# Kernel optimization log

Hardware: AMD Instinct MI355X
Metric: run time of the kernel (lower is better)

## Reference

```python
import jax, jax.numpy as jnp
import numpy as np

N = 100000   # n_nodes
E = 1600000  # n_edges (avg degree 16)
IN, HID, OUT = 128, 128, 64


def setup_inputs() -> dict:
    key = jax.random.key(0)
    k0, k1, k2, k3 = jax.random.split(key, 4)
    x = jax.random.normal(k0, (N, IN), dtype=jnp.float32)
    edge_index = jax.random.randint(k1, (2, E), 0, N, dtype=jnp.int32)
    # Glorot-ish init for GCNConv weights, zero bias (PyG default bias=True)
    W1 = jax.random.normal(k2, (IN, HID), dtype=jnp.float32) * (1.0 / np.sqrt(IN))
    b1 = jnp.zeros((HID,), dtype=jnp.float32)
    W2 = jax.random.normal(k3, (HID, OUT), dtype=jnp.float32) * (1.0 / np.sqrt(HID))
    b2 = jnp.zeros((OUT,), dtype=jnp.float32)
    return {"x": x, "W1": W1, "b1": b1, "W2": W2, "b2": b2, "edge_index": edge_index}


def gcn_layer(x, W, b, src, dst):
    """PyG GCNConv: add self-loops, symmetric deg^{-1/2} normalization,
    linear transform, scatter-add aggregation at dst, plus bias."""
    n = x.shape[0]
    h = x @ W                                   # [n, d_out]
    loops = jnp.arange(n, dtype=src.dtype)
    s = jnp.concatenate([src, loops])           # sources incl. self-loops
    d = jnp.concatenate([dst, loops])           # targets incl. self-loops
    deg = jax.ops.segment_sum(jnp.ones_like(d, dtype=h.dtype), d, num_segments=n)
    dinv = jnp.where(deg > 0, jax.lax.rsqrt(deg), 0.0)
    norm = dinv[s] * dinv[d]                    # [E+n]
    msg = h[s] * norm[:, None]                  # gather + scale
    out = jax.ops.segment_sum(msg, d, num_segments=n)  # scatter-add
    return out + b


def reference(x, W1, b1, W2, b2, edge_index):
    src, dst = edge_index[0], edge_index[1]
    h = jax.nn.relu(gcn_layer(x, W1, b1, src, dst))
    return gcn_layer(h, W2, b2, src, dst)
```

## Files before the change

kernel.cpp:

```cpp
#include <hip/hip_runtime.h>

#define NNODES 100000
#define NEDGES 1600000
#define IND 128
#define HIDD 128
#define OUTD 64

#define BSHIFT 9
#define BSIZE  512
#define NBUCK  ((NNODES + BSIZE - 1) / BSIZE)
#define HIST_EPB 8192
#define BIN_EPB  4096
#define SEG_CAP  10240

typedef unsigned int  uint32;
typedef unsigned short ushort16;
typedef __attribute__((ext_vector_type(8))) short short8;
typedef __attribute__((ext_vector_type(4))) float floatx4;

__device__ __forceinline__ unsigned short f2bf(float f) {
    union { float f; uint32 u; } x; x.f = f;
    uint32 u = x.u;
    return (unsigned short)((u + 0x7fffu + ((u >> 16) & 1u)) >> 16);
}
__device__ __forceinline__ float bflo(uint32 u) {
    union { uint32 i; float f; } x; x.i = u << 16; return x.f;
}
__device__ __forceinline__ float bfhi(uint32 u) {
    union { uint32 i; float f; } x; x.i = u & 0xffff0000u; return x.f;
}

__global__ void k_hist(const int* __restrict__ dst, int* __restrict__ bcounts, int e) {
    __shared__ int lh[NBUCK];
    for (int i = threadIdx.x; i < NBUCK; i += 256) lh[i] = 0;
    __syncthreads();
    int start = blockIdx.x * HIST_EPB;
    int end = min(start + HIST_EPB, e);
    for (int i = start + threadIdx.x; i < end; i += 256)
        atomicAdd(&lh[dst[i] >> BSHIFT], 1);
    __syncthreads();
    for (int i = threadIdx.x; i < NBUCK; i += 256)
        if (lh[i]) atomicAdd(&bcounts[i], lh[i]);
}

__global__ void k_bscan(const int* __restrict__ bcounts, int* __restrict__ boff,
                        int* __restrict__ bcur) {
    __shared__ int buf[256];
    const int tid = threadIdx.x;
    int v = (tid < NBUCK) ? bcounts[tid] : 0;
    buf[tid] = v;
    __syncthreads();
    for (int off = 1; off < 256; off <<= 1) {
        int t = (tid >= off) ? buf[tid - off] : 0;
        __syncthreads();
        buf[tid] += t;
        __syncthreads();
    }
    if (tid < NBUCK) { int ex = buf[tid] - v; boff[tid] = ex; bcur[tid] = ex; }
    if (tid == 255) boff[NBUCK] = buf[255];
}

__global__ void k_bin(const int* __restrict__ src, const int* __restrict__ dst,
                      int* __restrict__ bcur, uint32* __restrict__ staging, int e) {
    __shared__ int lh[NBUCK];
    __shared__ int lbase[NBUCK];
    __shared__ int lcur[NBUCK];
    __shared__ int gbase[NBUCK];
    __shared__ int sbuf[256];
    __shared__ uint2 lp[BIN_EPB];

    const int tid = threadIdx.x;
    for (int i = tid; i < NBUCK; i += 256) lh[i] = 0;
    __syncthreads();

    int start = blockIdx.x * BIN_EPB;
    int end = min(start + BIN_EPB, e);
    int n = end - start;

    for (int i = start + tid; i < end; i += 256)
        atomicAdd(&lh[dst[i] >> BSHIFT], 1);
    __syncthreads();

    int v = (tid < NBUCK) ? lh[tid] : 0;
    sbuf[tid] = v;
    __syncthreads();
    for (int off = 1; off < 256; off <<= 1) {
        int t = (tid >= off) ? sbuf[tid - off] : 0;
        __syncthreads();
        sbuf[tid] += t;
        __syncthreads();
    }
    if (tid < NBUCK) { int ex = sbuf[tid] - v; lbase[tid] = ex; lcur[tid] = ex; }
    __syncthreads();

    for (int i = start + tid; i < end; i += 256) {
        int d = dst[i], s = src[i];
        int b = d >> BSHIFT;
        int pos = atomicAdd(&lcur[b], 1);
        lp[pos] = make_uint2((uint32)s, (uint32)d);
    }
    if (tid < NBUCK) {
        int c = lh[tid];
        gbase[tid] = c ? atomicAdd(&bcur[tid], c) : 0;
    }
    __syncthreads();

    for (int i = tid; i < n; i += 256) {
        uint2 p = lp[i];
        int b = (int)(p.y >> BSHIFT);
        uint32 packed = ((p.y & (BSIZE - 1)) << 17) | p.x;
        staging[gbase[b] + (i - lbase[b])] = packed;
    }
}

__global__ void k_fill3(const uint32* __restrict__ staging, const int* __restrict__ boff,
                        int* __restrict__ row_ptr, int* __restrict__ csr_src,
                        float* __restrict__ dinv, int n) {
    __shared__ int nc[BSIZE];
    __shared__ int lcur[BSIZE];
    __shared__ int sbuf[256];
    __shared__ int seg[SEG_CAP];
    const int b = blockIdx.x;
    const int base = b << BSHIFT;
    const int tid = threadIdx.x;
    const int nn = min(BSIZE, n - base);

    for (int i = tid; i < BSIZE; i += 256) nc[i] = 0;
    __syncthreads();

    const int s0 = boff[b], s1 = boff[b + 1];
    for (int i = s0 + tid; i < s1; i += 256)
        atomicAdd(&nc[staging[i] >> 17], 1);
    __syncthreads();

    int a0 = nc[2 * tid], a1 = nc[2 * tid + 1];
    sbuf[tid] = a0 + a1;
    __syncthreads();
    for (int off = 1; off < 256; off <<= 1) {
        int t = (tid >= off) ? sbuf[tid - off] : 0;
        __syncthreads();
        sbuf[tid] += t;
        __syncthreads();
    }
    int ex = sbuf[tid] - (a0 + a1);
    const int r0 = s0;
    if (2 * tid < nn) {
        row_ptr[base + 2 * tid] = r0 + ex;
        dinv[base + 2 * tid] = rsqrtf((float)(a0 + 1));
    }
    if (2 * tid + 1 < nn) {
        row_ptr[base + 2 * tid + 1] = r0 + ex + a0;
        dinv[base + 2 * tid + 1] = rsqrtf((float)(a1 + 1));
    }
    lcur[2 * tid] = ex;
    lcur[2 * tid + 1] = ex + a0;
    if (b == (int)gridDim.x - 1 && tid == 255) row_ptr[n] = s1;
    __syncthreads();

    const int L = s1 - s0;
    for (int i = s0 + tid; i < s1; i += 256) {
        uint32 p = staging[i];
        int dl = (int)(p >> 17);
        int s  = (int)(p & 0x1FFFFu);
        int pos = atomicAdd(&lcur[dl], 1);
        if (pos < SEG_CAP) seg[pos] = s;
        else               csr_src[r0 + pos] = s;
    }
    __syncthreads();
    int lim = min(L, SEG_CAP);
    for (int i = tid; i < lim; i += 256) csr_src[r0 + i] = seg[i];
}

template<int K, int M>
__global__ void k_wt(const float* __restrict__ W, unsigned short* __restrict__ WT) {
    int idx = blockIdx.x * 256 + threadIdx.x;
    if (idx < K * M) {
        int k = idx / M, m = idx - k * M;
        WT[m * K + k] = f2bf(W[idx]);
    }
}

template<int K, int M>
__launch_bounds__(256)
__global__ void gemm_mfma(const float* __restrict__ A, const unsigned short* __restrict__ WT,
                          const float* __restrict__ dinv, unsigned short* __restrict__ C, int n) {
    constexpr int KP = K + 8;
    constexpr int NT = M / 16;
    __shared__ unsigned short Asl[64 * KP];
    __shared__ unsigned short Wsl[M * KP];

    const int tid = threadIdx.x;
    const int row0 = blockIdx.x * 64;

    {
        constexpr int SEG = (K * 2) / 16;
        const uint4* srcp = (const uint4*)WT;
        for (int idx = tid; idx < M * SEG; idx += 256) {
            int r = idx / SEG, s = idx - r * SEG;
            *(uint4*)(Wsl + r * KP + s * 8) = srcp[idx];
        }
    }
    {
        constexpr int F4R = K / 4;
        for (int idx = tid; idx < 64 * F4R; idx += 256) {
            int r = idx / F4R, s = idx - r * F4R;
            int grow = row0 + r; if (grow >= n) grow = n - 1;
            float4 v = *(const float4*)(A + (size_t)grow * K + s * 4);
            uint32 p0 = (uint32)f2bf(v.x) | ((uint32)f2bf(v.y) << 16);
            uint32 p1 = (uint32)f2bf(v.z) | ((uint32)f2bf(v.w) << 16);
            *(uint2*)(Asl + r * KP + s * 4) = make_uint2(p0, p1);
        }
    }
    __syncthreads();

    const int lane = tid & 63;
    const int wave = tid >> 6;
    const int mm = lane & 15;
    const int qq = lane >> 4;

    floatx4 acc[NT];
#pragma unroll
    for (int t = 0; t < NT; t++) acc[t] = (floatx4){0.f, 0.f, 0.f, 0.f};

#pragma unroll
    for (int kc = 0; kc < K / 32; kc++) {
        short8 a = *(const short8*)(Asl + (wave * 16 + mm) * KP + kc * 32 + qq * 8);
#pragma unroll
        for (int t = 0; t < NT; t++) {
            short8 b = *(const short8*)(Wsl + (t * 16 + mm) * KP + kc * 32 + qq * 8);
            acc[t] = __builtin_amdgcn_mfma_f32_16x16x32_bf16(a, b, acc[t], 0, 0, 0);
        }
    }

#pragma unroll
    for (int r = 0; r < 4; r++) {
        int grow = row0 + wave * 16 + qq * 4 + r;
        if (grow < n) {
            float dv = dinv[grow];
#pragma unroll
            for (int t = 0; t < NT; t++)
                C[(size_t)grow * M + t * 16 + mm] = f2bf(acc[t][r] * dv);
        }
    }
}

template<int M, bool RELU>
__launch_bounds__(256)
__global__ void gather_bf16(const ushort16* __restrict__ h,
                            const int* __restrict__ row_ptr,
                            const int* __restrict__ csr_src,
                            const float* __restrict__ dinv,
                            const float* __restrict__ bias,
                            float* __restrict__ outp, int n) {
    constexpr int LPG = M / 8;
    constexpr int GPB = 256 / LPG;
    const int g = threadIdx.x / LPG;
    const int l = threadIdx.x % LPG;
    const int v = blockIdx.x * GPB + g;
    if (v >= n) return;

    const float dv = dinv[v];
    float acc[8];

    {
        uint4 u = *(const uint4*)(h + (size_t)v * M + l * 8);
        acc[0] = bflo(u.x); acc[1] = bfhi(u.x);
        acc[2] = bflo(u.y); acc[3] = bfhi(u.y);
        acc[4] = bflo(u.z); acc[5] = bfhi(u.z);
        acc[6] = bflo(u.w); acc[7] = bfhi(u.w);
    }

    int j   = row_ptr[v];
    int end = row_ptr[v + 1];
    for (; j + 3 < end; j += 4) {
        int s0 = csr_src[j];
        int s1 = csr_src[j + 1];
        int s2 = csr_src[j + 2];
        int s3 = csr_src[j + 3];
        uint4 u0 = *(const uint4*)(h + (size_t)s0 * M + l * 8);
        uint4 u1 = *(const uint4*)(h + (size_t)s1 * M + l * 8);
        uint4 u2 = *(const uint4*)(h + (size_t)s2 * M + l * 8);
        uint4 u3 = *(const uint4*)(h + (size_t)s3 * M + l * 8);
        acc[0] += (bflo(u0.x) + bflo(u1.x)) + (bflo(u2.x) + bflo(u3.x));
        acc[1] += (bfhi(u0.x) + bfhi(u1.x)) + (bfhi(u2.x) + bfhi(u3.x));
        acc[2] += (bflo(u0.y) + bflo(u1.y)) + (bflo(u2.y) + bflo(u3.y));
        acc[3] += (bfhi(u0.y) + bfhi(u1.y)) + (bfhi(u2.y) + bfhi(u3.y));
        acc[4] += (bflo(u0.z) + bflo(u1.z)) + (bflo(u2.z) + bflo(u3.z));
        acc[5] += (bfhi(u0.z) + bfhi(u1.z)) + (bfhi(u2.z) + bfhi(u3.z));
        acc[6] += (bflo(u0.w) + bflo(u1.w)) + (bflo(u2.w) + bflo(u3.w));
        acc[7] += (bfhi(u0.w) + bfhi(u1.w)) + (bfhi(u2.w) + bfhi(u3.w));
    }
    for (; j < end; j++) {
        int s0 = csr_src[j];
        uint4 u0 = *(const uint4*)(h + (size_t)s0 * M + l * 8);
        acc[0] += bflo(u0.x); acc[1] += bfhi(u0.x);
        acc[2] += bflo(u0.y); acc[3] += bfhi(u0.y);
        acc[4] += bflo(u0.z); acc[5] += bfhi(u0.z);
        acc[6] += bflo(u0.w); acc[7] += bfhi(u0.w);
    }

#pragma unroll
    for (int i = 0; i < 8; i++) {
        acc[i] = acc[i] * dv + bias[l * 8 + i];
        if (RELU) acc[i] = fmaxf(acc[i], 0.0f);
    }
    float4 o0 = make_float4(acc[0], acc[1], acc[2], acc[3]);
    float4 o1 = make_float4(acc[4], acc[5], acc[6], acc[7]);
    float* op = outp + (size_t)v * M + l * 8;
    *(float4*)op = o0;
    *(float4*)(op + 4) = o1;
}

extern "C" void kernel_launch(void* const* d_in, const int* in_sizes, int n_in,
                              void* d_out, int out_size, void* d_ws, size_t ws_size,
                              hipStream_t stream) {
    const float* x  = (const float*)d_in[0];
    const float* W1 = (const float*)d_in[1];
    const float* b1 = (const float*)d_in[2];
    const float* W2 = (const float*)d_in[3];
    const float* b2 = (const float*)d_in[4];
    const int*   ei = (const int*)d_in[5];
    const int* src = ei;
    const int* dst = ei + NEDGES;
    float* out = (float*)d_out;

    char* ws = (char*)d_ws;
    float*  dinv    = (float*)ws;   ws += (size_t)NNODES * 4;
    int*    row_ptr = (int*)ws;     ws += (size_t)(NNODES + 4) * 4;
    int*    bcounts = (int*)ws;     ws += 256 * 4;
    int*    boff    = (int*)ws;     ws += 260 * 4;
    int*    bcur    = (int*)ws;     ws += 256 * 4;
    unsigned short* wt1 = (unsigned short*)ws;  ws += (size_t)IND * HIDD * 2;
    unsigned short* wt2 = (unsigned short*)ws;  ws += (size_t)HIDD * OUTD * 2;
    int*    csr_src = (int*)ws;     ws += (size_t)NEDGES * 4;
    uint32* staging = (uint32*)ws;  ws += (size_t)NEDGES * 4;
    float*  hr      = (float*)ws;   ws += (size_t)NNODES * HIDD * 4;
    ushort16* hbf   = (ushort16*)ws;

    hipMemsetAsync(bcounts, 0, NBUCK * 4, stream);
    k_hist<<<(NEDGES + HIST_EPB - 1) / HIST_EPB, 256, 0, stream>>>(dst, bcounts, NEDGES);
    k_bscan<<<1, 256, 0, stream>>>(bcounts, boff, bcur);
    k_bin<<<(NEDGES + BIN_EPB - 1) / BIN_EPB, 256, 0, stream>>>(src, dst, bcur, staging, NEDGES);
    k_fill3<<<NBUCK, 256, 0, stream>>>(staging, boff, row_ptr, csr_src, dinv, NNODES);

    k_wt<IND, HIDD><<<(IND * HIDD + 255) / 256, 256, 0, stream>>>(W1, wt1);
    k_wt<HIDD, OUTD><<<(HIDD * OUTD + 255) / 256, 256, 0, stream>>>(W2, wt2);

    gemm_mfma<IND, HIDD><<<(NNODES + 63) / 64, 256, 0, stream>>>(
        x, wt1, dinv, (unsigned short*)hbf, NNODES);
    gather_bf16<HIDD, true><<<(NNODES * (HIDD / 8) + 255) / 256, 256, 0, stream>>>(
        hbf, row_ptr, csr_src, dinv, b1, hr, NNODES);

    gemm_mfma<HIDD, OUTD><<<(NNODES + 63) / 64, 256, 0, stream>>>(
        hr, wt2, dinv, (unsigned short*)hbf, NNODES);
    gather_bf16<OUTD, false><<<(NNODES * (OUTD / 8) + 255) / 256, 256, 0, stream>>>(
        hbf, row_ptr, csr_src, dinv, b2, out, NNODES);
}
```

Before: 331.0 us.

## Degree-sort gather nodes, store hidden layer in bf16, unroll gather by 8

```diff
diff --git a/kernel.cpp b/kernel.cpp
--- a/kernel.cpp
+++ b/kernel.cpp
@@ -14,7 +14,6 @@
 #define SEG_CAP  10240
 
 typedef unsigned int  uint32;
-typedef unsigned short ushort16;
 typedef __attribute__((ext_vector_type(8))) short short8;
 typedef __attribute__((ext_vector_type(4))) float floatx4;
 
@@ -115,10 +114,11 @@
 
 __global__ void k_fill3(const uint32* __restrict__ staging, const int* __restrict__ boff,
                         int* __restrict__ row_ptr, int* __restrict__ csr_src,
-                        float* __restrict__ dinv, int n) {
+                        float* __restrict__ dinv, int* __restrict__ dhist, int n) {
     __shared__ int nc[BSIZE];
     __shared__ int lcur[BSIZE];
     __shared__ int sbuf[256];
+    __shared__ int dh[64];
     __shared__ int seg[SEG_CAP];
     const int b = blockIdx.x;
     const int base = b << BSHIFT;
@@ -126,6 +126,7 @@
     const int nn = min(BSIZE, n - base);
 
     for (int i = tid; i < BSIZE; i += 256) nc[i] = 0;
+    if (tid < 64) dh[tid] = 0;
     __syncthreads();
 
     const int s0 = boff[b], s1 = boff[b + 1];
@@ -147,15 +148,19 @@
     if (2 * tid < nn) {
         row_ptr[base + 2 * tid] = r0 + ex;
         dinv[base + 2 * tid] = rsqrtf((float)(a0 + 1));
+        atomicAdd(&dh[min(a0, 63)], 1);
     }
     if (2 * tid + 1 < nn) {
         row_ptr[base + 2 * tid + 1] = r0 + ex + a0;
         dinv[base + 2 * tid + 1] = rsqrtf((float)(a1 + 1));
+        atomicAdd(&dh[min(a1, 63)], 1);
     }
     lcur[2 * tid] = ex;
     lcur[2 * tid + 1] = ex + a0;
     if (b == (int)gridDim.x - 1 && tid == 255) row_ptr[n] = s1;
     __syncthreads();
+
+    if (tid < 64 && dh[tid]) atomicAdd(&dhist[tid], dh[tid]);
 
     const int L = s1 - s0;
     for (int i = s0 + tid; i < s1; i += 256) {
@@ -171,18 +176,58 @@
     for (int i = tid; i < lim; i += 256) csr_src[r0 + i] = seg[i];
 }
 
-template<int K, int M>
-__global__ void k_wt(const float* __restrict__ W, unsigned short* __restrict__ WT) {
+__global__ void k_dscan(const int* __restrict__ dhist, int* __restrict__ dcur) {
+    __shared__ int buf[64];
+    const int tid = threadIdx.x;
+    int v = dhist[tid];
+    buf[tid] = v;
+    __syncthreads();
+    for (int off = 1; off < 64; off <<= 1) {
+        int t = (tid >= off) ? buf[tid - off] : 0;
+        __syncthreads();
+        buf[tid] += t;
+        __syncthreads();
+    }
+    dcur[tid] = buf[tid] - v;
+}
+
+__global__ void k_dperm(const int* __restrict__ row_ptr, int* __restrict__ dcur,
+                        int* __restrict__ perm, int n) {
+    __shared__ int lh[64], gbase[64];
+    const int tid = threadIdx.x;
+    if (tid < 64) lh[tid] = 0;
+    __syncthreads();
+    int v = blockIdx.x * 256 + tid;
+    int deg = 0, lpos = 0;
+    bool valid = v < n;
+    if (valid) {
+        deg = min(row_ptr[v + 1] - row_ptr[v], 63);
+        lpos = atomicAdd(&lh[deg], 1);
+    }
+    __syncthreads();
+    if (tid < 64) gbase[tid] = lh[tid] ? atomicAdd(&dcur[tid], lh[tid]) : 0;
+    __syncthreads();
+    if (valid) perm[gbase[deg] + lpos] = v;
+}
+
+__global__ void k_wt_both(const float* __restrict__ W1, const float* __restrict__ W2,
+                          unsigned short* __restrict__ wt1, unsigned short* __restrict__ wt2) {
     int idx = blockIdx.x * 256 + threadIdx.x;
-    if (idx < K * M) {
-        int k = idx / M, m = idx - k * M;
-        WT[m * K + k] = f2bf(W[idx]);
-    }
-}
-
-template<int K, int M>
+    if (idx < IND * HIDD) {
+        int k = idx / HIDD, m = idx - k * HIDD;
+        wt1[m * IND + k] = f2bf(W1[idx]);
+    } else {
+        int j = idx - IND * HIDD;
+        if (j < HIDD * OUTD) {
+            int k = j / OUTD, m = j - k * OUTD;
+            wt2[m * HIDD + k] = f2bf(W2[j]);
+        }
+    }
+}
+
+template<int K, int M, bool ABF16>
 __launch_bounds__(256)
-__global__ void gemm_mfma(const float* __restrict__ A, const unsigned short* __restrict__ WT,
+__global__ void gemm_mfma(const void* __restrict__ Ap, const unsigned short* __restrict__ WT,
                           const float* __restrict__ dinv, unsigned short* __restrict__ C, int n) {
     constexpr int KP = K + 8;
     constexpr int NT = M / 16;
@@ -200,12 +245,21 @@
             *(uint4*)(Wsl + r * KP + s * 8) = srcp[idx];
         }
     }
-    {
+    if constexpr (ABF16) {
+        constexpr int U4R = K / 8;
+        const unsigned short* Ab = (const unsigned short*)Ap;
+        for (int idx = tid; idx < 64 * U4R; idx += 256) {
+            int r = idx / U4R, s = idx - r * U4R;
+            int grow = row0 + r; if (grow >= n) grow = n - 1;
+            *(uint4*)(Asl + r * KP + s * 8) = *(const uint4*)(Ab + (size_t)grow * K + s * 8);
+        }
+    } else {
         constexpr int F4R = K / 4;
+        const float* Af = (const float*)Ap;
         for (int idx = tid; idx < 64 * F4R; idx += 256) {
             int r = idx / F4R, s = idx - r * F4R;
             int grow = row0 + r; if (grow >= n) grow = n - 1;
-            float4 v = *(const float4*)(A + (size_t)grow * K + s * 4);
+            float4 v = *(const float4*)(Af + (size_t)grow * K + s * 4);
             uint32 p0 = (uint32)f2bf(v.x) | ((uint32)f2bf(v.y) << 16);
             uint32 p1 = (uint32)f2bf(v.z) | ((uint32)f2bf(v.w) << 16);
             *(uint2*)(Asl + r * KP + s * 4) = make_uint2(p0, p1);
@@ -244,24 +298,25 @@
     }
 }
 
-template<int M, bool RELU>
+template<int M, bool RELU, bool OBF16>
 __launch_bounds__(256)
-__global__ void gather_bf16(const ushort16* __restrict__ h,
-                            const int* __restrict__ row_ptr,
-                            const int* __restrict__ csr_src,
-                            const float* __restrict__ dinv,
-                            const float* __restrict__ bias,
-                            float* __restrict__ outp, int n) {
+__global__ void gather_k(const unsigned short* __restrict__ h,
+                         const int* __restrict__ row_ptr,
+                         const int* __restrict__ csr_src,
+                         const int* __restrict__ perm,
+                         const float* __restrict__ dinv,
+                         const float* __restrict__ bias,
+                         void* __restrict__ outp, int n) {
     constexpr int LPG = M / 8;
     constexpr int GPB = 256 / LPG;
     const int g = threadIdx.x / LPG;
     const int l = threadIdx.x % LPG;
-    const int v = blockIdx.x * GPB + g;
-    if (v >= n) return;
+    const int gi = blockIdx.x * GPB + g;
+    if (gi >= n) return;
+    const int v = perm[gi];
 
     const float dv = dinv[v];
     float acc[8];
-
     {
         uint4 u = *(const uint4*)(h + (size_t)v * M + l * 8);
         acc[0] = bflo(u.x); acc[1] = bfhi(u.x);
@@ -272,23 +327,20 @@
 
     int j   = row_ptr[v];
     int end = row_ptr[v + 1];
-    for (; j + 3 < end; j += 4) {
-        int s0 = csr_src[j];
-        int s1 = csr_src[j + 1];
-        int s2 = csr_src[j + 2];
-        int s3 = csr_src[j + 3];
-        uint4 u0 = *(const uint4*)(h + (size_t)s0 * M + l * 8);
-        uint4 u1 = *(const uint4*)(h + (size_t)s1 * M + l * 8);
-        uint4 u2 = *(const uint4*)(h + (size_t)s2 * M + l * 8);
-        uint4 u3 = *(const uint4*)(h + (size_t)s3 * M + l * 8);
-        acc[0] += (bflo(u0.x) + bflo(u1.x)) + (bflo(u2.x) + bflo(u3.x));
-        acc[1] += (bfhi(u0.x) + bfhi(u1.x)) + (bfhi(u2.x) + bfhi(u3.x));
-        acc[2] += (bflo(u0.y) + bflo(u1.y)) + (bflo(u2.y) + bflo(u3.y));
-        acc[3] += (bfhi(u0.y) + bfhi(u1.y)) + (bfhi(u2.y) + bfhi(u3.y));
-        acc[4] += (bflo(u0.z) + bflo(u1.z)) + (bflo(u2.z) + bflo(u3.z));
-        acc[5] += (bfhi(u0.z) + bfhi(u1.z)) + (bfhi(u2.z) + bfhi(u3.z));
-        acc[6] += (bflo(u0.w) + bflo(u1.w)) + (bflo(u2.w) + bflo(u3.w));
-        acc[7] += (bfhi(u0.w) + bfhi(u1.w)) + (bfhi(u2.w) + bfhi(u3.w));
+    for (; j + 7 < end; j += 8) {
+        int s[8];
+#pragma unroll
+        for (int k = 0; k < 8; k++) s[k] = csr_src[j + k];
+        uint4 u[8];
+#pragma unroll
+        for (int k = 0; k < 8; k++) u[k] = *(const uint4*)(h + (size_t)s[k] * M + l * 8);
+#pragma unroll
+        for (int k = 0; k < 8; k++) {
+            acc[0] += bflo(u[k].x); acc[1] += bfhi(u[k].x);
+            acc[2] += bflo(u[k].y); acc[3] += bfhi(u[k].y);
+            acc[4] += bflo(u[k].z); acc[5] += bfhi(u[k].z);
+            acc[6] += bflo(u[k].w); acc[7] += bfhi(u[k].w);
+        }
     }
     for (; j < end; j++) {
         int s0 = csr_src[j];
@@ -304,11 +356,18 @@
         acc[i] = acc[i] * dv + bias[l * 8 + i];
         if (RELU) acc[i] = fmaxf(acc[i], 0.0f);
     }
-    float4 o0 = make_float4(acc[0], acc[1], acc[2], acc[3]);
-    float4 o1 = make_float4(acc[4], acc[5], acc[6], acc[7]);
-    float* op = outp + (size_t)v * M + l * 8;
-    *(float4*)op = o0;
-    *(float4*)(op + 4) = o1;
+
+    if constexpr (OBF16) {
+        uint32 p[4];
+#pragma unroll
+        for (int c = 0; c < 4; c++)
+            p[c] = (uint32)f2bf(acc[2 * c]) | ((uint32)f2bf(acc[2 * c + 1]) << 16);
+        *(uint4*)((unsigned short*)outp + (size_t)v * M + l * 8) = make_uint4(p[0], p[1], p[2], p[3]);
+    } else {
+        float* op = (float*)outp + (size_t)v * M + l * 8;
+        *(float4*)op = make_float4(acc[0], acc[1], acc[2], acc[3]);
+        *(float4*)(op + 4) = make_float4(acc[4], acc[5], acc[6], acc[7]);
+    }
 }
 
 extern "C" void kernel_launch(void* const* d_in, const int* in_sizes, int n_in,
@@ -328,31 +387,35 @@
     float*  dinv    = (float*)ws;   ws += (size_t)NNODES * 4;
     int*    row_ptr = (int*)ws;     ws += (size_t)(NNODES + 4) * 4;
     int*    bcounts = (int*)ws;     ws += 256 * 4;
+    int*    dhist   = (int*)ws;     ws += 64 * 4;
     int*    boff    = (int*)ws;     ws += 260 * 4;
     int*    bcur    = (int*)ws;     ws += 256 * 4;
+    int*    dcur    = (int*)ws;     ws += 64 * 4;
+    int*    perm    = (int*)ws;     ws += (size_t)NNODES * 4;
     unsigned short* wt1 = (unsigned short*)ws;  ws += (size_t)IND * HIDD * 2;
     unsigned short* wt2 = (unsigned short*)ws;  ws += (size_t)HIDD * OUTD * 2;
     int*    csr_src = (int*)ws;     ws += (size_t)NEDGES * 4;
     uint32* staging = (uint32*)ws;  ws += (size_t)NEDGES * 4;
-    float*  hr      = (float*)ws;   ws += (size_t)NNODES * HIDD * 4;
-    ushort16* hbf   = (ushort16*)ws;
-
-    hipMemsetAsync(bcounts, 0, NBUCK * 4, stream);
+    unsigned short* hr  = (unsigned short*)ws;  ws += (size_t)NNODES * HIDD * 2;
+    unsigned short* hbf = (unsigned short*)ws;
+
+    hipMemsetAsync(bcounts, 0, (256 + 64) * 4, stream);
     k_hist<<<(NEDGES + HIST_EPB - 1) / HIST_EPB, 256, 0, stream>>>(dst, bcounts, NEDGES);
     k_bscan<<<1, 256, 0, stream>>>(bcounts, boff, bcur);
     k_bin<<<(NEDGES + BIN_EPB - 1) / BIN_EPB, 256, 0, stream>>>(src, dst, bcur, staging, NEDGES);
-    k_fill3<<<NBUCK, 256, 0, stream>>>(staging, boff, row_ptr, csr_src, dinv, NNODES);
-
-    k_wt<IND, HIDD><<<(IND * HIDD + 255) / 256, 256, 0, stream>>>(W1, wt1);
-    k_wt<HIDD, OUTD><<<(HIDD * OUTD + 255) / 256, 256, 0, stream>>>(W2, wt2);
-
-    gemm_mfma<IND, HIDD><<<(NNODES + 63) / 64, 256, 0, stream>>>(
-        x, wt1, dinv, (unsigned short*)hbf, NNODES);
-    gather_bf16<HIDD, true><<<(NNODES * (HIDD / 8) + 255) / 256, 256, 0, stream>>>(
-        hbf, row_ptr, csr_src, dinv, b1, hr, NNODES);
-
-    gemm_mfma<HIDD, OUTD><<<(NNODES + 63) / 64, 256, 0, stream>>>(
-        hr, wt2, dinv, (unsigned short*)hbf, NNODES);
-    gather_bf16<OUTD, false><<<(NNODES * (OUTD / 8) + 255) / 256, 256, 0, stream>>>(
-        hbf, row_ptr, csr_src, dinv, b2, out, NNODES);
-}
+    k_fill3<<<NBUCK, 256, 0, stream>>>(staging, boff, row_ptr, csr_src, dinv, dhist, NNODES);
+    k_dscan<<<1, 64, 0, stream>>>(dhist, dcur);
+    k_dperm<<<(NNODES + 255) / 256, 256, 0, stream>>>(row_ptr, dcur, perm, NNODES);
+
+    k_wt_both<<<(IND * HIDD + HIDD * OUTD + 255) / 256, 256, 0, stream>>>(W1, W2, wt1, wt2);
+
+    gemm_mfma<IND, HIDD, false><<<(NNODES + 63) / 64, 256, 0, stream>>>(
+        x, wt1, dinv, hbf, NNODES);
+    gather_k<HIDD, true, true><<<(NNODES * (HIDD / 8) + 255) / 256, 256, 0, stream>>>(
+        hbf, row_ptr, csr_src, perm, dinv, b1, hr, NNODES);
+
+    gemm_mfma<HIDD, OUTD, true><<<(NNODES + 63) / 64, 256, 0, stream>>>(
+        hr, wt2, dinv, hbf, NNODES);
+    gather_k<OUTD, false, false><<<(NNODES * (OUTD / 8) + 255) / 256, 256, 0, stream>>>(
+        hbf, row_ptr, csr_src, perm, dinv, b2, out, NNODES);
+}
```

Result: slower. 339.9 us (+2.7%).
